# Performance work log

Hardware: AMD Instinct MI355X
Metric: run time of the kernel (lower is better)

The kernel has to match this reference:

```python
import jax, jax.numpy as jnp
import numpy as np


def setup_inputs() -> dict:
    key = jax.random.key(0)
    k1, k2, k3, k4 = jax.random.split(key, 4)
    b, n1, n2, h = 8, 2048, 2048, 1024
    scale = 1.0 / np.sqrt(h)
    return {
        "S1": jax.random.normal(k1, (b, n1, h), dtype=jnp.float32),
        "S2": jax.random.normal(k2, (b, n2, h), dtype=jnp.float32),
        "W1": jax.random.normal(k3, (h, h), dtype=jnp.float32) * scale,
        "W2": jax.random.normal(k4, (h, h), dtype=jnp.float32) * scale,
    }


def reference(S1, S2, W1, W2):
    # nn.Linear(h, h, bias=False): y = x @ W.T
    S2_h = jnp.einsum('bnh,kh->bnk', S2, W1)            # (b, N2, h)
    scores1 = jnp.einsum('bmh,bnh->bmn', S1, S2_h)      # (b, N1, N2)
    attn1 = jax.nn.softmax(scores1, axis=-1)
    S1_out = jnp.einsum('bmn,bnh->bmh', attn1, S2)      # (b, N1, h)

    S1_h = jnp.einsum('bmh,kh->bmk', S1, W2)            # (b, N1, h)
    scores2 = jnp.einsum('bnh,bmh->bnm', S2, S1_h)      # (b, N2, N1)
    attn2 = jax.nn.softmax(scores2, axis=-1)
    S2_out = jnp.einsum('bnm,bmh->bnh', attn2, S1)      # (b, N2, h)
    return (S1_out, S2_out)
```

## Files before the change

kernel.cpp:

```cpp
#include <hip/hip_runtime.h>

typedef _Float16 f16;
typedef _Float16 f16x4 __attribute__((ext_vector_type(4)));
typedef _Float16 f16x8 __attribute__((ext_vector_type(8)));
typedef float    f32x4 __attribute__((ext_vector_type(4)));

#define MFMA(a,b,c) __builtin_amdgcn_mfma_f32_16x16x32_f16(a,b,c,0,0,0)
#define SBAR() __builtin_amdgcn_sched_barrier(0)
#define BARRIER() do { SBAR(); __builtin_amdgcn_s_barrier(); SBAR(); } while (0)
#define VMCNT(n) do { SBAR(); asm volatile("s_waitcnt vmcnt(" #n ")" ::: "memory"); SBAR(); } while (0)
#define LGKM0() do { asm volatile("s_waitcnt lgkmcnt(0)" ::: "memory"); SBAR(); } while (0)

__device__ __forceinline__ void gload_lds16(const f16* g, f16* l) {
  __builtin_amdgcn_global_load_lds(
      (const __attribute__((address_space(1))) unsigned int*)g,
      (__attribute__((address_space(3))) unsigned int*)l, 16, 0, 0);
}

__global__ __launch_bounds__(256)
void tof16_kernel(const float* __restrict__ x, f16* __restrict__ y, int n4) {
  int i = blockIdx.x * 256 + threadIdx.x;
  if (i >= n4) return;
  f32x4 v = ((const f32x4*)x)[i];
  f16x4 h;
#pragma unroll
  for (int j = 0; j < 4; j++) h[j] = (f16)v[j];
  ((f16x4*)y)[i] = h;
}

__global__ __launch_bounds__(256)
void prep_f16_kernel(const float* __restrict__ in, f16* __restrict__ rm,
                     f16* __restrict__ tr) {
  __shared__ f16 t[64][68];
  const int tid = threadIdx.x;
  const size_t z = blockIdx.z;
  const int n0 = blockIdx.x * 64, h0 = blockIdx.y * 64;
  const int rr = tid >> 4, cc = (tid & 15) * 4;
#pragma unroll
  for (int p = 0; p < 4; p++) {
    int n = rr + p * 16;
    f32x4 v = *(const f32x4*)(in + ((size_t)z * 2048 + n0 + n) * 1024 + h0 + cc);
    f16x4 h;
#pragma unroll
    for (int j = 0; j < 4; j++) h[j] = (f16)v[j];
    *(f16x4*)&t[n][cc] = h;
    *(f16x4*)(rm + ((size_t)z * 2048 + n0 + n) * 1024 + h0 + cc) = h;
  }
  __syncthreads();
#pragma unroll
  for (int p = 0; p < 4; p++) {
    int h = rr + p * 16;
    f16x4 o;
#pragma unroll
    for (int j = 0; j < 4; j++) o[j] = t[cc + j][h];
    *(f16x4*)(tr + ((size_t)z * 1024 + h0 + h) * 2048 + n0 + cc) = o;
  }
}

template <int OUTF32>
__global__ __launch_bounds__(512, 2)
void gemm256(const f16* __restrict__ Ag, size_t zA,
             const f16* __restrict__ Bg, size_t zB,
             void* __restrict__ Cg, size_t zC,
             int lda, int ldb, int ldc, int K, int ZB, int gx) {
  __shared__ f16 sm[8][8192];
  const int tid = threadIdx.x;
  const int id = blockIdx.x;
  const size_t z = id % ZB;
  const int k = id / ZB;
  const int bx = k % gx, by = k / gx;
  const f16* A = Ag + z * zA + (size_t)bx * 256 * lda;
  const f16* B = Bg + z * zB + (size_t)by * 256 * ldb;

  const int lane = tid & 63, w = tid >> 6;
  const int wm = w >> 2, wn = w & 3;
  const int lr = lane & 15, kg = lane >> 4;
  const int sx = (kg ^ ((lr >> 1) & 3)) << 3;
  const int aoff = wm * 4096 + lr * 32 + sx;
  const int boff = wn * 2048 + lr * 32 + sx;
  const int colx = (((tid & 3) ^ ((tid >> 3) & 3)) << 3);
  const int srow = tid >> 2;
  const int wls = w * 512;

  f32x4 acc[8][4] = {};
  f16x8 af[8], bf0, bf1;

#define STAGE(cc, mat, kkv, ktc) do {                                          \
    const f16* gs = ((mat) ? B : A) + (size_t)srow * ((mat) ? ldb : lda) +     \
                    (ktc) + (kkv) * 32 + colx;                                 \
    f16* ls = &sm[(cc) * 4 + (mat) * 2 + (kkv)][wls];                          \
    gload_lds16(gs, ls);                                                       \
    gload_lds16(gs + (size_t)128 * ((mat) ? ldb : lda), ls + 4096);            \
  } while (0)

#define LOAD_A(cc, kkv) do { _Pragma("unroll")                                 \
    for (int fm = 0; fm < 8; fm++)                                             \
      af[fm] = *(const f16x8*)&sm[(cc) * 4 + (kkv)][aoff + fm * 512];          \
  } while (0)

#define LOAD_B(cc, kkv, nh) do {                                               \
    bf0 = *(const f16x8*)&sm[(cc) * 4 + 2 + (kkv)][boff + (nh) * 1024];        \
    bf1 = *(const f16x8*)&sm[(cc) * 4 + 2 + (kkv)][boff + (nh) * 1024 + 512];  \
  } while (0)

#define DOMFMA(nh) do {                                                        \
    __builtin_amdgcn_s_setprio(1);                                             \
    _Pragma("unroll")                                                          \
    for (int fm = 0; fm < 8; fm++) {                                           \
      acc[fm][(nh) * 2]     = MFMA(af[fm], bf0, acc[fm][(nh) * 2]);            \
      acc[fm][(nh) * 2 + 1] = MFMA(af[fm], bf1, acc[fm][(nh) * 2 + 1]);        \
    }                                                                          \
    __builtin_amdgcn_s_setprio(0);                                             \
    SBAR();                                                                    \
  } while (0)

  const int nt = K >> 6;
  STAGE(0, 0, 0, 0);
  STAGE(0, 1, 0, 0);
  STAGE(0, 0, 1, 0);
  STAGE(0, 1, 1, 0);
  VMCNT(4);
  BARRIER();

  for (int t = 0; t < nt - 1; ++t) {
    const int c = t & 1;
    const int kt1 = (t + 1) << 6;
    LOAD_A(c, 0); LOAD_B(c, 0, 0);
    STAGE(c ^ 1, 0, 0, kt1);
    BARRIER();
    LGKM0();
    DOMFMA(0);
    BARRIER();
    LOAD_B(c, 0, 1);
    STAGE(c ^ 1, 1, 0, kt1);
    BARRIER();
    LGKM0();
    DOMFMA(1);
    VMCNT(4);
    BARRIER();
    LOAD_A(c, 1); LOAD_B(c, 1, 0);
    STAGE(c ^ 1, 0, 1, kt1);
    BARRIER();
    LGKM0();
    DOMFMA(0);
    BARRIER();
    LOAD_B(c, 1, 1);
    STAGE(c ^ 1, 1, 1, kt1);
    BARRIER();
    LGKM0();
    DOMFMA(1);
    VMCNT(4);
    BARRIER();
  }
  {
    const int c = (nt - 1) & 1;
    LOAD_A(c, 0); LOAD_B(c, 0, 0);
    BARRIER();
    LGKM0();
    DOMFMA(0);
    BARRIER();
    LOAD_B(c, 0, 1);
    BARRIER();
    LGKM0();
    DOMFMA(1);
    VMCNT(0);
    BARRIER();
    LOAD_A(c, 1); LOAD_B(c, 1, 0);
    BARRIER();
    LGKM0();
    DOMFMA(0);
    BARRIER();
    LOAD_B(c, 1, 1);
    BARRIER();
    LGKM0();
    DOMFMA(1);
  }

#pragma unroll
  for (int fm = 0; fm < 8; fm++)
#pragma unroll
    for (int fn = 0; fn < 4; fn++)
#pragma unroll
      for (int q = 0; q < 4; q++) {
        size_t grow = (size_t)bx * 256 + wm * 128 + fm * 16 + kg * 4 + q;
        int gcol = by * 256 + wn * 64 + fn * 16 + lr;
        if (OUTF32)
          ((float*)Cg)[z * zC + grow * ldc + gcol] = acc[fm][fn][q];
        else
          ((f16*)Cg)[z * zC + grow * ldc + gcol] = (f16)acc[fm][fn][q];
      }
#undef STAGE
#undef LOAD_A
#undef LOAD_B
#undef DOMFMA
}

__global__ __launch_bounds__(256)
void softmax_rows(const float* __restrict__ SC, f16* __restrict__ Pb) {
  const float* r = SC + (size_t)blockIdx.x * 2048;
  f16* po = Pb + (size_t)blockIdx.x * 2048;
  const int tid = threadIdx.x;
  f32x4 a = *(const f32x4*)(r + tid * 8);
  f32x4 b = *(const f32x4*)(r + tid * 8 + 4);
  float x[8] = {a[0], a[1], a[2], a[3], b[0], b[1], b[2], b[3]};
#pragma unroll
  for (int i = 0; i < 8; i++) x[i] = fminf(fmaxf(x[i], -1e30f), 1e30f);
  float m = x[0];
#pragma unroll
  for (int i = 1; i < 8; i++) m = fmaxf(m, x[i]);
#pragma unroll
  for (int off = 32; off; off >>= 1) m = fmaxf(m, __shfl_xor(m, off));
  __shared__ float rmax[4], rsum[4];
  const int w = tid >> 6, lane = tid & 63;
  if (!lane) rmax[w] = m;
  __syncthreads();
  m = fmaxf(fmaxf(rmax[0], rmax[1]), fmaxf(rmax[2], rmax[3]));
  float e[8], s = 0.f;
#pragma unroll
  for (int i = 0; i < 8; i++) {
    e[i] = __expf(x[i] - m);
    s += e[i];
  }
#pragma unroll
  for (int off = 32; off; off >>= 1) s += __shfl_xor(s, off);
  if (!lane) rsum[w] = s;
  __syncthreads();
  s = rsum[0] + rsum[1] + rsum[2] + rsum[3];
  float inv = 1.0f / s;
  f16x8 p;
#pragma unroll
  for (int i = 0; i < 8; i++) p[i] = (f16)(e[i] * inv);
  *(f16x8*)(po + tid * 8) = p;
}

extern "C" void kernel_launch(void* const* d_in, const int* in_sizes, int n_in,
                              void* d_out, int out_size, void* d_ws, size_t ws_size,
                              hipStream_t stream) {
  const float* S1 = (const float*)d_in[0];
  const float* S2 = (const float*)d_in[1];
  const float* W1 = (const float*)d_in[2];
  const float* W2 = (const float*)d_in[3];
  float* out = (float*)d_out;
  const int B = 8, N = 2048, H = 1024;
  const size_t NH = (size_t)N * H;
  const size_t WN = (size_t)H * H;

  char* ws = (char*)d_ws;
  f16* W1h = (f16*)ws;
  f16* W2h = W1h + WN;
  size_t fixed = 2 * WN * sizeof(f16);
  size_t perb = 5 * NH * sizeof(f16) + (size_t)N * N * sizeof(float) +
                (size_t)N * N * sizeof(f16);

  int bc = 1;
  const int cands[4] = {8, 4, 2, 1};
  for (int ci = 0; ci < 4; ci++) {
    if (fixed + (size_t)cands[ci] * perb <= ws_size) { bc = cands[ci]; break; }
  }
  f16* Ah = (f16*)(ws + fixed);
  f16* Bh = Ah + (size_t)bc * NH;
  f16* At = Bh + (size_t)bc * NH;
  f16* Bt = At + (size_t)bc * NH;
  f16* Kh = Bt + (size_t)bc * NH;
  float* SC = (float*)(Kh + (size_t)bc * NH);
  f16* Pb = (f16*)(SC + (size_t)bc * N * N);

  {
    int n4 = (int)(WN / 4);
    tof16_kernel<<<dim3((n4 + 255) / 256), 256, 0, stream>>>(W1, W1h, n4);
    tof16_kernel<<<dim3((n4 + 255) / 256), 256, 0, stream>>>(W2, W2h, n4);
  }

  for (int c0 = 0; c0 < B; c0 += bc) {
    prep_f16_kernel<<<dim3(N / 64, H / 64, bc), 256, 0, stream>>>(
        S1 + (size_t)c0 * NH, Ah, At);
    prep_f16_kernel<<<dim3(N / 64, H / 64, bc), 256, 0, stream>>>(
        S2 + (size_t)c0 * NH, Bh, Bt);

    for (int path = 0; path < 2; path++) {
      const f16* Qh = path ? Bh : Ah;
      const f16* Xh = path ? Ah : Bh;
      const f16* Vt = path ? At : Bt;
      const f16* Wh = path ? W2h : W1h;
      float* Op = out + (size_t)path * B * NH + (size_t)c0 * NH;

      gemm256<0><<<dim3(bc * 8 * 4), 512, 0, stream>>>(
          Xh, 0, Wh, 0, Kh, 0, H, H, H, H, 1, bc * 8);
      gemm256<1><<<dim3(bc * 64), 512, 0, stream>>>(
          Qh, NH, Kh, NH, SC, (size_t)N * N, H, H, N, H, bc, 8);
      softmax_rows<<<dim3(bc * N), 256, 0, stream>>>(SC, Pb);
      gemm256<1><<<dim3(bc * 32), 512, 0, stream>>>(
          Pb, (size_t)N * N, Vt, NH, Op, NH, N, N, H, N, bc, 8);
    }
  }
}
```

Measured before the change: 502.6 us.

## Batch both attention paths and all batches into single GEMM and softmax launches

When the workspace is large enough, both cross-attention paths and all 8 batches go through one launch per stage: projection, scores, softmax and PV. This replaces the per-chunk, per-path loop. The GEMM kernel gains a path index with dual A/B base pointers and an XCD-aware block-to-tile mapping, so blocks sharing operands land on the same XCD. The fp32 outputs are written with nontemporal stores. The aim is to fill all CUs with larger grids and cut launch count, at the cost of a much larger workspace (two full score matrices), with the old loop kept as a fallback.

```diff
diff --git a/kernel.cpp b/kernel.cpp
--- a/kernel.cpp
+++ b/kernel.cpp
@@ -57,20 +57,31 @@
   }
 }
 
-template <int OUTF32>
+template <int OUTF32, int MAP>
 __global__ __launch_bounds__(512, 2)
-void gemm256(const f16* __restrict__ Ag, size_t zA,
-             const f16* __restrict__ Bg, size_t zB,
+void gemm256(const f16* __restrict__ A0g, const f16* __restrict__ A1g, size_t zA,
+             const f16* __restrict__ B0g, const f16* __restrict__ B1g, size_t zB,
              void* __restrict__ Cg, size_t zC,
-             int lda, int ldb, int ldc, int K, int ZB, int gx) {
+             int lda, int ldb, int ldc, int K, int P1, int gx) {
   __shared__ f16 sm[8][8192];
   const int tid = threadIdx.x;
   const int id = blockIdx.x;
-  const size_t z = id % ZB;
-  const int k = id / ZB;
-  const int bx = k % gx, by = k / gx;
-  const f16* A = Ag + z * zA + (size_t)bx * 256 * lda;
-  const f16* B = Bg + z * zB + (size_t)by * 256 * ldb;
+  int u, k, bx, by;
+  if (MAP == 0) {
+    const int xcd = id & 7, step = id >> 3;
+    u = xcd + 8 * (step >> P1);
+    k = step & ((1 << P1) - 1);
+    bx = k & 7;
+    by = k >> 3;
+  } else {
+    u = id % P1;
+    k = id / P1;
+    bx = k % gx;
+    by = k / gx;
+  }
+  const int path = u >> 3, z = u & 7;
+  const f16* A = (path ? A1g : A0g) + (size_t)z * zA + (size_t)bx * 256 * lda;
+  const f16* B = (path ? B1g : B0g) + (size_t)z * zB + (size_t)by * 256 * ldb;
 
   const int lane = tid & 63, w = tid >> 6;
   const int wm = w >> 2, wn = w & 3;
@@ -184,10 +195,13 @@
       for (int q = 0; q < 4; q++) {
         size_t grow = (size_t)bx * 256 + wm * 128 + fm * 16 + kg * 4 + q;
         int gcol = by * 256 + wn * 64 + fn * 16 + lr;
-        if (OUTF32)
-          ((float*)Cg)[z * zC + grow * ldc + gcol] = acc[fm][fn][q];
-        else
-          ((f16*)Cg)[z * zC + grow * ldc + gcol] = (f16)acc[fm][fn][q];
+        if (OUTF32) {
+          __builtin_nontemporal_store(
+              acc[fm][fn][q],
+              &((float*)Cg)[(size_t)u * zC + grow * ldc + gcol]);
+        } else {
+          ((f16*)Cg)[(size_t)u * zC + grow * ldc + gcol] = (f16)acc[fm][fn][q];
+        }
       }
 #undef STAGE
 #undef LOAD_A
@@ -243,15 +257,46 @@
   float* out = (float*)d_out;
   const int B = 8, N = 2048, H = 1024;
   const size_t NH = (size_t)N * H;
+  const size_t NN = (size_t)N * N;
   const size_t WN = (size_t)H * H;
 
   char* ws = (char*)d_ws;
   f16* W1h = (f16*)ws;
   f16* W2h = W1h + WN;
   size_t fixed = 2 * WN * sizeof(f16);
-  size_t perb = 5 * NH * sizeof(f16) + (size_t)N * N * sizeof(float) +
-                (size_t)N * N * sizeof(f16);
-
+
+  size_t needA = fixed + 4 * (8 * NH) * sizeof(f16) + 16 * NH * sizeof(f16) +
+                 16 * NN * sizeof(float) + 16 * NN * sizeof(f16);
+
+  {
+    int n4 = (int)(WN / 4);
+    tof16_kernel<<<dim3((n4 + 255) / 256), 256, 0, stream>>>(W1, W1h, n4);
+    tof16_kernel<<<dim3((n4 + 255) / 256), 256, 0, stream>>>(W2, W2h, n4);
+  }
+
+  if (ws_size >= needA) {
+    f16* Ah = (f16*)(ws + fixed);
+    f16* Bh = Ah + 8 * NH;
+    f16* At = Bh + 8 * NH;
+    f16* Bt = At + 8 * NH;
+    f16* Kh = Bt + 8 * NH;
+    float* SC = (float*)(Kh + 16 * NH);
+    f16* Pb = (f16*)(SC + 16 * NN);
+
+    prep_f16_kernel<<<dim3(N / 64, H / 64, B), 256, 0, stream>>>(S1, Ah, At);
+    prep_f16_kernel<<<dim3(N / 64, H / 64, B), 256, 0, stream>>>(S2, Bh, Bt);
+
+    gemm256<0, 0><<<dim3(512), 512, 0, stream>>>(
+        Bh, Ah, NH, W1h, W2h, 0, Kh, NH, H, H, H, H, 5, 8);
+    gemm256<1, 0><<<dim3(1024), 512, 0, stream>>>(
+        Ah, Bh, NH, Kh, Kh + 8 * NH, NH, SC, NN, H, H, N, H, 6, 8);
+    softmax_rows<<<dim3(16 * N), 256, 0, stream>>>(SC, Pb);
+    gemm256<1, 0><<<dim3(512), 512, 0, stream>>>(
+        Pb, Pb + 8 * NN, NN, Bt, At, NH, out, NH, N, N, H, N, 5, 8);
+    return;
+  }
+
+  size_t perb = 5 * NH * sizeof(f16) + NN * sizeof(float) + NN * sizeof(f16);
   int bc = 1;
   const int cands[4] = {8, 4, 2, 1};
   for (int ci = 0; ci < 4; ci++) {
@@ -263,34 +308,26 @@
   f16* Bt = At + (size_t)bc * NH;
   f16* Kh = Bt + (size_t)bc * NH;
   float* SC = (float*)(Kh + (size_t)bc * NH);
-  f16* Pb = (f16*)(SC + (size_t)bc * N * N);
-
-  {
-    int n4 = (int)(WN / 4);
-    tof16_kernel<<<dim3((n4 + 255) / 256), 256, 0, stream>>>(W1, W1h, n4);
-    tof16_kernel<<<dim3((n4 + 255) / 256), 256, 0, stream>>>(W2, W2h, n4);
-  }
+  f16* Pb = (f16*)(SC + (size_t)bc * NN);
 
   for (int c0 = 0; c0 < B; c0 += bc) {
     prep_f16_kernel<<<dim3(N / 64, H / 64, bc), 256, 0, stream>>>(
         S1 + (size_t)c0 * NH, Ah, At);
     prep_f16_kernel<<<dim3(N / 64, H / 64, bc), 256, 0, stream>>>(
         S2 + (size_t)c0 * NH, Bh, Bt);
-
     for (int path = 0; path < 2; path++) {
       const f16* Qh = path ? Bh : Ah;
       const f16* Xh = path ? Ah : Bh;
       const f16* Vt = path ? At : Bt;
       const f16* Wh = path ? W2h : W1h;
       float* Op = out + (size_t)path * B * NH + (size_t)c0 * NH;
-
-      gemm256<0><<<dim3(bc * 8 * 4), 512, 0, stream>>>(
-          Xh, 0, Wh, 0, Kh, 0, H, H, H, H, 1, bc * 8);
-      gemm256<1><<<dim3(bc * 64), 512, 0, stream>>>(
-          Qh, NH, Kh, NH, SC, (size_t)N * N, H, H, N, H, bc, 8);
+      gemm256<0, 1><<<dim3(bc * 32), 512, 0, stream>>>(
+          Xh, Xh, 0, Wh, Wh, 0, Kh, 0, H, H, H, H, 1, bc * 8);
+      gemm256<1, 1><<<dim3(bc * 64), 512, 0, stream>>>(
+          Qh, Qh, NH, Kh, Kh, NH, SC, NN, H, H, N, H, bc, 8);
       softmax_rows<<<dim3(bc * N), 256, 0, stream>>>(SC, Pb);
-      gemm256<1><<<dim3(bc * 32), 512, 0, stream>>>(
-          Pb, (size_t)N * N, Vt, NH, Op, NH, N, N, H, N, bc, 8);
+      gemm256<1, 1><<<dim3(bc * 32), 512, 0, stream>>>(
+          Pb, Pb, NN, Vt, Vt, NH, Op, NH, N, N, H, N, bc, 8);
     }
   }
 }
```

After: 543.0 us. 1.08x slower.
